# Optimization experiments

Hardware: AMD Instinct MI355X
Metric: run time of the kernel (lower is better)

The kernel has to match this reference:

```python
import jax, jax.numpy as jnp
import numpy as np

N_NODES = 50000
N_EDGES = 1600000
SLOPE = 0.01  # torch leaky_relu default negative_slope


def _lrelu(x):
    return jnp.where(x >= 0, x, SLOPE * x)


def _graph_conv(x, edge_index, w_rel, b_rel, w_root):
    # PyG GraphConv (aggr='add'): out_i = W_rel @ sum_{j->i} x_j + b_rel + W_root @ x_i
    src, dst = edge_index[0], edge_index[1]
    agg = jax.ops.segment_sum(x[src], dst, num_segments=x.shape[0])  # [N, F_in]
    return agg @ w_rel.T + b_rel + x @ w_root.T


def setup_inputs() -> dict:
    key = jax.random.key(0)
    ks = jax.random.split(key, 12)

    def glorot(k, shape):
        fan_in = shape[-1]
        return jax.random.normal(k, shape, dtype=jnp.float32) / np.sqrt(fan_in)

    x = jax.random.normal(ks[0], (N_NODES, 2048), dtype=jnp.float32)
    edge_index = jax.random.randint(ks[1], (2, N_EDGES), 0, N_NODES, dtype=jnp.int64)

    return {
        "x": x,
        "edge_index": edge_index,
        "lin1_w": glorot(ks[2], (128, 2048)),
        "lin1_b": jnp.zeros((128,), jnp.float32),
        "conv1_w_rel": glorot(ks[3], (64, 128)),
        "conv1_b_rel": jnp.zeros((64,), jnp.float32),
        "conv1_w_root": glorot(ks[4], (64, 128)),
        "conv4_w_rel": glorot(ks[5], (32, 64)),
        "conv4_b_rel": jnp.zeros((32,), jnp.float32),
        "conv4_w_root": glorot(ks[6], (32, 64)),
        "pos_w": glorot(ks[7], (3, 32)),
        "pos_b": jnp.zeros((3,), jnp.float32),
    }


def reference(x, edge_index, lin1_w, lin1_b, conv1_w_rel, conv1_b_rel,
              conv1_w_root, conv4_w_rel, conv4_b_rel, conv4_w_root,
              pos_w, pos_b):
    # dropout layers are identity at inference
    h = _lrelu(x @ lin1_w.T + lin1_b)                                  # [N, 128]
    h = _lrelu(_graph_conv(h, edge_index, conv1_w_rel, conv1_b_rel, conv1_w_root))  # [N, 64]
    h = _lrelu(_graph_conv(h, edge_index, conv4_w_rel, conv4_b_rel, conv4_w_root))  # [N, 32]
    position = h @ pos_w.T + pos_b                                     # [N, 3]
    return position
```

## Files before the change

### kernel.cpp

```cpp
#include <hip/hip_runtime.h>

#define N_NODES 50000
#define N_EDGES 1600000
#define LIN_BLOCKS 782
#define HIST_BLOCKS 1024

typedef __attribute__((ext_vector_type(4))) float f32x4;
typedef __attribute__((ext_vector_type(8))) short bf16x8;
typedef unsigned short u16;

__device__ __forceinline__ float lrelu(float x) { return x >= 0.f ? x : 0.01f * x; }

__device__ __forceinline__ u16 f2bf(float f) {
    union { float f; unsigned u; } v; v.f = f;
    unsigned u = v.u;
    u += 0x7fffu + ((u >> 16) & 1u);
    return (u16)(u >> 16);
}

__device__ __forceinline__ float bf2f(u16 v) {
    union { unsigned u; float f; } x; x.u = ((unsigned)v) << 16; return x.f;
}

__device__ __forceinline__ bf16x8 cvt8(float4 a, float4 b) {
    bf16x8 r;
    r[0] = (short)f2bf(a.x); r[1] = (short)f2bf(a.y);
    r[2] = (short)f2bf(a.z); r[3] = (short)f2bf(a.w);
    r[4] = (short)f2bf(b.x); r[5] = (short)f2bf(b.y);
    r[6] = (short)f2bf(b.z); r[7] = (short)f2bf(b.w);
    return r;
}

__launch_bounds__(256)
__global__ void k_prep(const float* __restrict__ W1,
                       const float* __restrict__ W2a, const float* __restrict__ W2b,
                       const float* __restrict__ W3a, const float* __restrict__ W3b,
                       u16* __restrict__ wf1, u16* __restrict__ wf2, u16* __restrict__ wf3,
                       const int* __restrict__ ei, int* __restrict__ deg)
{
    const int b = blockIdx.x;
    if (b < 1024) {
        int i = b * 256 + threadIdx.x;
        int e = i & 7, lane = (i >> 3) & 63, nf = (i >> 9) & 7, ks = i >> 12;
        int n = nf * 16 + (lane & 15);
        int k = ks * 32 + 8 * (lane >> 4) + e;
        wf1[i] = f2bf(W1[(size_t)n * 2048 + k]);
    } else if (b < 1088) {
        int i = (b - 1024) * 256 + threadIdx.x;
        int e = i & 7, lane = (i >> 3) & 63, nf = (i >> 9) & 7, ks = i >> 12;
        int n = nf * 16 + (lane & 15);
        int k = ks * 32 + 8 * (lane >> 4) + e;
        float v = (n < 64) ? W2a[(size_t)n * 128 + k] : W2b[(size_t)(n - 64) * 128 + k];
        wf2[i] = f2bf(v);
    } else if (b < 1104) {
        int i = (b - 1088) * 256 + threadIdx.x;
        int e = i & 7, lane = (i >> 3) & 63, nf = (i >> 9) & 3, ks = i >> 11;
        int n = nf * 16 + (lane & 15);
        int k = ks * 32 + 8 * (lane >> 4) + e;
        float v = (n < 32) ? W3a[(size_t)n * 64 + k] : W3b[(size_t)(n - 32) * 64 + k];
        wf3[i] = f2bf(v);
    } else {
        for (int e = (b - 1104) * 256 + threadIdx.x; e < N_EDGES; e += HIST_BLOCKS * 256)
            atomicAdd(deg + ei[N_EDGES + e], 1);
    }
}

__device__ __forceinline__ void wr_stage(char* slot, int aw0, int aw1, int bw,
                                         float4 A0, float4 A1, float4 B0, float4 B1)
{
    *(float4*)(slot + aw0) = A0;
    *(float4*)(slot + aw1) = A1;
    *(float4*)(slot + bw) = B0;
    *(float4*)(slot + bw + 16) = B1;
}

__device__ __forceinline__ void compute_step(const char* slot, int lane, int wave,
                                             f32x4 acc[8])
{
    const int lrow = lane & 15, lgrp = lane >> 4;
    const int row = wave * 16 + lrow;
    const int swz = (row & 7) << 4;
    const char* Ab = slot + row * 128;
    float4 a0 = *(const float4*)(Ab + ((lgrp * 32) ^ swz));
    float4 a1 = *(const float4*)(Ab + ((lgrp * 32 + 16) ^ swz));
    bf16x8 af = cvt8(a0, a1);
    const char* Bb = slot + 8192 + lane * 16;
    __builtin_amdgcn_s_setprio(1);
#pragma unroll
    for (int nf = 0; nf < 8; nf++) {
        bf16x8 bf = *(const bf16x8*)(Bb + nf * 1024);
        acc[nf] = __builtin_amdgcn_mfma_f32_16x16x32_bf16(af, bf, acc[nf], 0, 0, 0);
    }
    __builtin_amdgcn_s_setprio(0);
}

__launch_bounds__(256, 3)
__global__ void k_linf(const float* __restrict__ X, const u16* __restrict__ Wf1,
                       const u16* __restrict__ Wf2,
                       const float* __restrict__ Bv, const float* __restrict__ brel,
                       u16* __restrict__ t1, float* __restrict__ acc1,
                       const int* __restrict__ ei, int* __restrict__ cur,
                       int* __restrict__ csr)
{
    __shared__ __align__(16) char lds[2][16384];
    __shared__ __align__(16) u16 hlbuf[4][2048];

    const int t = threadIdx.x, wave = t >> 6, lane = t & 63;
    const int lrow = lane & 15, lgrp = lane >> 4;
    const int m0 = blockIdx.x * 64;

    const int arow_l = t >> 2, q = t & 3;
    int grow = m0 + arow_l; if (grow >= N_NODES) grow = N_NODES - 1;
    const float4* ap = (const float4*)(X + (size_t)grow * 2048);
    const float4* bp = (const float4*)Wf1;
    const int aw0 = arow_l * 128 + (((q * 2 + 0) ^ (arow_l & 7)) << 4);
    const int aw1 = arow_l * 128 + (((q * 2 + 1) ^ (arow_l & 7)) << 4);
    const int bw = 8192 + t * 32;

    f32x4 acc[8];
#pragma unroll
    for (int i = 0; i < 8; i++) acc[i] = (f32x4)0.f;

    float4 cA0 = ap[q * 2], cA1 = ap[q * 2 + 1];
    float4 cB0 = bp[t * 2], cB1 = bp[t * 2 + 1];
    float4 nA0 = ap[8 + q * 2], nA1 = ap[8 + q * 2 + 1];
    float4 nB0 = bp[512 + t * 2], nB1 = bp[512 + t * 2 + 1];
    wr_stage(lds[0], aw0, aw1, bw, cA0, cA1, cB0, cB1);
    asm volatile("s_waitcnt lgkmcnt(0)" ::: "memory");
    __builtin_amdgcn_s_barrier();
    __builtin_amdgcn_sched_barrier(0);

#pragma unroll 2
    for (int s = 0; s < 62; s++) {
        float4 fA0 = ap[(s + 2) * 8 + q * 2], fA1 = ap[(s + 2) * 8 + q * 2 + 1];
        float4 fB0 = bp[(s + 2) * 512 + t * 2], fB1 = bp[(s + 2) * 512 + t * 2 + 1];

        compute_step(lds[s & 1], lane, wave, acc);
        __builtin_amdgcn_s_barrier();
        __builtin_amdgcn_sched_barrier(0);

        wr_stage(lds[(s + 1) & 1], aw0, aw1, bw, nA0, nA1, nB0, nB1);
        asm volatile("s_waitcnt lgkmcnt(0)" ::: "memory");
        __builtin_amdgcn_s_barrier();
        __builtin_amdgcn_sched_barrier(0);

        nA0 = fA0; nA1 = fA1; nB0 = fB0; nB1 = fB1;
    }
    compute_step(lds[0], lane, wave, acc);
    __builtin_amdgcn_s_barrier();
    __builtin_amdgcn_sched_barrier(0);
    wr_stage(lds[1], aw0, aw1, bw, nA0, nA1, nB0, nB1);
    asm volatile("s_waitcnt lgkmcnt(0)" ::: "memory");
    __builtin_amdgcn_s_barrier();
    __builtin_amdgcn_sched_barrier(0);
    compute_step(lds[1], lane, wave, acc);

    u16* hl = hlbuf[wave];
#pragma unroll
    for (int nf = 0; nf < 8; nf++) {
        const int col = nf * 16 + lrow;
        const float bias = Bv[col];
#pragma unroll
        for (int r = 0; r < 4; r++) {
            const int row = lgrp * 4 + r;
            hl[row * 128 + (((col >> 3) ^ (row & 7)) << 3) + (col & 7)] =
                f2bf(lrelu(acc[nf][r] + bias));
        }
    }
    bf16x8 af2[4];
#pragma unroll
    for (int ks = 0; ks < 4; ks++)
        af2[ks] = *(const bf16x8*)(hl + lrow * 128 + ((((ks << 2) + lgrp) ^ (lrow & 7)) << 3));

    f32x4 dacc[8];
#pragma unroll
    for (int i = 0; i < 8; i++) dacc[i] = (f32x4)0.f;
    const u16* bp2 = Wf2 + lane * 8;
#pragma unroll
    for (int ks = 0; ks < 4; ks++) {
#pragma unroll
        for (int nf = 0; nf < 8; nf++) {
            bf16x8 bf = *(const bf16x8*)(bp2 + ks * 4096 + nf * 512);
            dacc[nf] = __builtin_amdgcn_mfma_f32_16x16x32_bf16(af2[ks], bf, dacc[nf], 0, 0, 0);
        }
    }

    const int rbase = m0 + wave * 16 + lgrp * 4;
#pragma unroll
    for (int nf = 0; nf < 8; nf++) {
        const int col = nf * 16 + lrow;
#pragma unroll
        for (int r = 0; r < 4; r++) {
            const int row = rbase + r;
            if (row < N_NODES) {
                if (col < 64) t1[(size_t)row * 64 + col] = f2bf(dacc[nf][r]);
                else          acc1[(size_t)row * 64 + (col - 64)] = dacc[nf][r] + brel[col - 64];
            }
        }
    }

    for (int e = blockIdx.x * 256 + t; e < N_EDGES; e += LIN_BLOCKS * 256) {
        const int dst = ei[N_EDGES + e];
        const int p = atomicAdd(cur + dst, 1);
        csr[p] = ei[e];
    }
}

__launch_bounds__(256, 2)
__global__ void k_dualf2(const float* __restrict__ A, const u16* __restrict__ Wf,
                         const float* __restrict__ brel,
                         u16* __restrict__ t2, float* __restrict__ acc2)
{
    const int t = threadIdx.x, wave = t >> 6, lane = t & 63;
    const int lrow = lane & 15, lgrp = lane >> 4;
    const int arow = blockIdx.x * 64 + wave * 16 + lrow;
    const float* ap = A + (size_t)(arow < N_NODES ? arow : 0) * 64 + 8 * lgrp;
    const u16* bp = Wf + lane * 8;

    float4 a00 = *(const float4*)(ap + 0);
    float4 a01 = *(const float4*)(ap + 4);
    float4 a10 = *(const float4*)(ap + 32);
    float4 a11 = *(const float4*)(ap + 36);

    f32x4 acc[4];
#pragma unroll
    for (int i = 0; i < 4; i++) acc[i] = (f32x4)0.f;

    a00.x = lrelu(a00.x); a00.y = lrelu(a00.y); a00.z = lrelu(a00.z); a00.w = lrelu(a00.w);
    a01.x = lrelu(a01.x); a01.y = lrelu(a01.y); a01.z = lrelu(a01.z); a01.w = lrelu(a01.w);
    bf16x8 af0 = cvt8(a00, a01);
    a10.x = lrelu(a10.x); a10.y = lrelu(a10.y); a10.z = lrelu(a10.z); a10.w = lrelu(a10.w);
    a11.x = lrelu(a11.x); a11.y = lrelu(a11.y); a11.z = lrelu(a11.z); a11.w = lrelu(a11.w);
    bf16x8 af1 = cvt8(a10, a11);

#pragma unroll
    for (int nf = 0; nf < 4; nf++) {
        bf16x8 b0 = *(const bf16x8*)(bp + nf * 512);
        bf16x8 b1 = *(const bf16x8*)(bp + 2048 + nf * 512);
        acc[nf] = __builtin_amdgcn_mfma_f32_16x16x32_bf16(af0, b0, acc[nf], 0, 0, 0);
        acc[nf] = __builtin_amdgcn_mfma_f32_16x16x32_bf16(af1, b1, acc[nf], 0, 0, 0);
    }

    const int rbase = blockIdx.x * 64 + wave * 16 + lgrp * 4;
#pragma unroll
    for (int nf = 0; nf < 4; nf++) {
        const int col = nf * 16 + lrow;
#pragma unroll
        for (int r = 0; r < 4; r++) {
            const int row = rbase + r;
            if (row < N_NODES) {
                if (col < 32) t2[(size_t)row * 32 + col] = f2bf(acc[nf][r]);
                else          acc2[(size_t)row * 32 + (col - 32)] = acc[nf][r] + brel[col - 32];
            }
        }
    }
}

__launch_bounds__(256)
__global__ void k_scan1(const int* __restrict__ deg, int* __restrict__ tmp,
                        int* __restrict__ bsum)
{
    __shared__ int sm[256];
    const int tid = threadIdx.x;
    const int i = blockIdx.x * 256 + tid;
    int d = (i < N_NODES) ? deg[i] : 0;
    sm[tid] = d;
    __syncthreads();
#pragma unroll
    for (int off = 1; off < 256; off <<= 1) {
        int v = (tid >= off) ? sm[tid - off] : 0;
        __syncthreads();
        sm[tid] += v;
        __syncthreads();
    }
    if (i < N_NODES) tmp[i] = sm[tid];
    if (tid == 255) bsum[blockIdx.x] = sm[255];
}

__launch_bounds__(256)
__global__ void k_scan2p(const int* __restrict__ bsum, int* __restrict__ boff, int nb)
{
    __shared__ int sm[256];
    const int tid = threadIdx.x;
    int v = (tid < nb) ? bsum[tid] : 0;
    sm[tid] = v;
    __syncthreads();
#pragma unroll
    for (int off = 1; off < 256; off <<= 1) {
        int u = (tid >= off) ? sm[tid - off] : 0;
        __syncthreads();
        sm[tid] += u;
        __syncthreads();
    }
    if (tid < nb) boff[tid] = sm[tid] - v;
}

__launch_bounds__(256)
__global__ void k_scan3(const int* __restrict__ tmp, const int* __restrict__ boff,
                        const int* __restrict__ deg, int* __restrict__ ro,
                        int* __restrict__ cur)
{
    const int i = blockIdx.x * 256 + threadIdx.x;
    if (i < N_NODES) {
        int incl = tmp[i] + boff[i >> 8];
        ro[i + 1] = incl;
        cur[i] = incl - deg[i];
    }
    if (i == 0) ro[0] = 0;
}

__launch_bounds__(256)
__global__ void k_gather64(const int* __restrict__ ro, const int* __restrict__ csr,
                           const u16* __restrict__ t, float* __restrict__ acc)
{
    const int wid = (blockIdx.x << 2) | (threadIdx.x >> 6);
    if (wid >= N_NODES) return;
    const int lane = threadIdx.x & 63;
    const int s = ro[wid], e = ro[wid + 1];
    float a = acc[(size_t)wid * 64 + lane];
    int i = s;
    for (; i + 8 <= e; i += 8) {
        int s0 = csr[i], s1 = csr[i + 1], s2 = csr[i + 2], s3 = csr[i + 3];
        int s4 = csr[i + 4], s5 = csr[i + 5], s6 = csr[i + 6], s7 = csr[i + 7];
        u16 v0 = t[(size_t)s0 * 64 + lane], v1 = t[(size_t)s1 * 64 + lane];
        u16 v2 = t[(size_t)s2 * 64 + lane], v3 = t[(size_t)s3 * 64 + lane];
        u16 v4 = t[(size_t)s4 * 64 + lane], v5 = t[(size_t)s5 * 64 + lane];
        u16 v6 = t[(size_t)s6 * 64 + lane], v7 = t[(size_t)s7 * 64 + lane];
        a += bf2f(v0); a += bf2f(v1); a += bf2f(v2); a += bf2f(v3);
        a += bf2f(v4); a += bf2f(v5); a += bf2f(v6); a += bf2f(v7);
    }
    for (; i < e; ++i) a += bf2f(t[(size_t)csr[i] * 64 + lane]);
    acc[(size_t)wid * 64 + lane] = a;
}

__launch_bounds__(256)
__global__ void k_gpos(const int* __restrict__ ro, const int* __restrict__ csr,
                       const u16* __restrict__ t, const float* __restrict__ acc2,
                       const float* __restrict__ PW, const float* __restrict__ PB,
                       float* __restrict__ out)
{
    const int wid = (blockIdx.x << 2) | (threadIdx.x >> 6);
    if (wid >= N_NODES) return;
    const int lane = threadIdx.x & 63;
    const int half = lane >> 5, f = lane & 31;
    const int s = ro[wid], e = ro[wid + 1];
    float a = 0.f;
    int i = s;
    for (; i + 8 <= e; i += 8) {
        int s0 = csr[i + half], s1 = csr[i + 2 + half];
        int s2 = csr[i + 4 + half], s3 = csr[i + 6 + half];
        u16 v0 = t[(size_t)s0 * 32 + f], v1 = t[(size_t)s1 * 32 + f];
        u16 v2 = t[(size_t)s2 * 32 + f], v3 = t[(size_t)s3 * 32 + f];
        a += bf2f(v0); a += bf2f(v1); a += bf2f(v2); a += bf2f(v3);
    }
    for (; i < e; i += 2) {
        int idx = i + half;
        if (idx < e) a += bf2f(t[(size_t)csr[idx] * 32 + f]);
    }
    a += __shfl_xor(a, 32, 64);

    float v = lrelu(acc2[(size_t)wid * 32 + f] + a);
    float p0 = v * PW[f], p1 = v * PW[32 + f], p2 = v * PW[64 + f];
#pragma unroll
    for (int off = 16; off >= 1; off >>= 1) {
        p0 += __shfl_xor(p0, off, 64);
        p1 += __shfl_xor(p1, off, 64);
        p2 += __shfl_xor(p2, off, 64);
    }
    if (lane == 0) {
        out[(size_t)wid * 3 + 0] = p0 + PB[0];
        out[(size_t)wid * 3 + 1] = p1 + PB[1];
        out[(size_t)wid * 3 + 2] = p2 + PB[2];
    }
}

extern "C" void kernel_launch(void* const* d_in, const int* in_sizes, int n_in,
                              void* d_out, int out_size, void* d_ws, size_t ws_size,
                              hipStream_t stream)
{
    const float* x        = (const float*)d_in[0];
    const int*   ei       = (const int*)d_in[1];
    const float* lin1_w   = (const float*)d_in[2];
    const float* lin1_b   = (const float*)d_in[3];
    const float* c1_wrel  = (const float*)d_in[4];
    const float* c1_brel  = (const float*)d_in[5];
    const float* c1_wroot = (const float*)d_in[6];
    const float* c4_wrel  = (const float*)d_in[7];
    const float* c4_brel  = (const float*)d_in[8];
    const float* c4_wroot = (const float*)d_in[9];
    const float* pos_w    = (const float*)d_in[10];
    const float* pos_b    = (const float*)d_in[11];
    float* out = (float*)d_out;

    char* base = (char*)d_ws;
    u16*   t1b  = (u16*)base;
    float* acc1 = (float*)(base + 6400000);
    u16*   t2b  = (u16*)(base + 19200000);
    float* acc2 = (float*)(base + 22400000);
    u16*   wf1  = (u16*)(base + 28800000);
    u16*   wf2  = wf1 + 262144;
    u16*   wf3  = wf2 + 16384;
    int*   ibase = (int*)(wf3 + 4096);
    const int NPAD = ((N_NODES + 255) / 256) * 256;
    int* deg  = ibase;
    int* tmp  = deg  + NPAD;
    int* ro   = tmp  + NPAD;
    int* cur  = ro   + NPAD;
    int* bsum = cur  + NPAD;
    int* boff = bsum + 256;
    int* csr  = boff + 256;
    const int NB = (N_NODES + 255) / 256;

    hipMemsetAsync(deg, 0, (size_t)NPAD * sizeof(int), stream);
    hipLaunchKernelGGL(k_prep, dim3(1104 + HIST_BLOCKS), dim3(256), 0, stream,
                       lin1_w, c1_wrel, c1_wroot, c4_wrel, c4_wroot,
                       wf1, wf2, wf3, ei, deg);
    hipLaunchKernelGGL(k_scan1, dim3(NB), dim3(256), 0, stream, deg, tmp, bsum);
    hipLaunchKernelGGL(k_scan2p, dim3(1), dim3(256), 0, stream, bsum, boff, NB);
    hipLaunchKernelGGL(k_scan3, dim3(NB), dim3(256), 0, stream, tmp, boff, deg, ro, cur);

    hipLaunchKernelGGL(k_linf, dim3(LIN_BLOCKS), dim3(256), 0, stream,
                       x, wf1, wf2, lin1_b, c1_brel, t1b, acc1, ei, cur, csr);
    hipLaunchKernelGGL(k_gather64, dim3((N_NODES + 3) / 4), dim3(256), 0, stream,
                       ro, csr, t1b, acc1);
    hipLaunchKernelGGL(k_dualf2, dim3((N_NODES + 63) / 64), dim3(256), 0, stream,
                       acc1, wf3, c4_brel, t2b, acc2);
    hipLaunchKernelGGL(k_gpos, dim3((N_NODES + 3) / 4), dim3(256), 0, stream,
                       ro, csr, t2b, acc2, pos_w, pos_b, out);
}
```

Before: 369.7 us.

## Stage bf16 operands in LDS and retile waves to 32x64 output blocks

The first GEMM now converts X tiles to bf16 before writing them to LDS, and copies the pre-converted bf16 weights into LDS as-is rather than as float. This halves LDS footprint per stage and moves the conversion out of the compute step. Each wave now computes a 32x64 sub-tile (2 A fragments by 4 B fragments) instead of 16x128, which cuts per-wave B-fragment LDS reads. The epilogue reuses the staging LDS for the hidden tile, with an extra barrier since waves exchange rows. Lower LDS use allows raising launch bounds occupancy from 3 to 4 blocks.

After: 361.4 us. 1.02x faster.

```diff
diff --git a/kernel.cpp b/kernel.cpp
--- a/kernel.cpp
+++ b/kernel.cpp
@@ -65,36 +65,35 @@
     }
 }
 
-__device__ __forceinline__ void wr_stage(char* slot, int aw0, int aw1, int bw,
-                                         float4 A0, float4 A1, float4 B0, float4 B1)
-{
-    *(float4*)(slot + aw0) = A0;
-    *(float4*)(slot + aw1) = A1;
-    *(float4*)(slot + bw) = B0;
-    *(float4*)(slot + bw + 16) = B1;
-}
-
 __device__ __forceinline__ void compute_step(const char* slot, int lane, int wave,
-                                             f32x4 acc[8])
-{
-    const int lrow = lane & 15, lgrp = lane >> 4;
-    const int row = wave * 16 + lrow;
-    const int swz = (row & 7) << 4;
-    const char* Ab = slot + row * 128;
-    float4 a0 = *(const float4*)(Ab + ((lgrp * 32) ^ swz));
-    float4 a1 = *(const float4*)(Ab + ((lgrp * 32 + 16) ^ swz));
-    bf16x8 af = cvt8(a0, a1);
-    const char* Bb = slot + 8192 + lane * 16;
+                                             f32x4 acc[2][4])
+{
+    const int lrow = lane & 15;
+    const int k16 = lane >> 4;
+    const int nfb = (wave >> 1) << 2;
+    const int rb = (wave & 1) << 5;
+
+    bf16x8 af[2];
+#pragma unroll
+    for (int st = 0; st < 2; st++) {
+        const int row = rb + st * 16 + lrow;
+        af[st] = *(const bf16x8*)(slot + row * 64 + ((k16 ^ (row & 3)) << 4));
+    }
+    bf16x8 bf[4];
+#pragma unroll
+    for (int j = 0; j < 4; j++)
+        bf[j] = *(const bf16x8*)(slot + 4096 + (nfb + j) * 1024 + lane * 16);
+
     __builtin_amdgcn_s_setprio(1);
 #pragma unroll
-    for (int nf = 0; nf < 8; nf++) {
-        bf16x8 bf = *(const bf16x8*)(Bb + nf * 1024);
-        acc[nf] = __builtin_amdgcn_mfma_f32_16x16x32_bf16(af, bf, acc[nf], 0, 0, 0);
-    }
+    for (int st = 0; st < 2; st++)
+#pragma unroll
+        for (int j = 0; j < 4; j++)
+            acc[st][j] = __builtin_amdgcn_mfma_f32_16x16x32_bf16(af[st], bf[j], acc[st][j], 0, 0, 0);
     __builtin_amdgcn_s_setprio(0);
 }
 
-__launch_bounds__(256, 3)
+__launch_bounds__(256, 4)
 __global__ void k_linf(const float* __restrict__ X, const u16* __restrict__ Wf1,
                        const u16* __restrict__ Wf2,
                        const float* __restrict__ Bv, const float* __restrict__ brel,
@@ -102,44 +101,49 @@
                        const int* __restrict__ ei, int* __restrict__ cur,
                        int* __restrict__ csr)
 {
-    __shared__ __align__(16) char lds[2][16384];
-    __shared__ __align__(16) u16 hlbuf[4][2048];
+    __shared__ __align__(16) char lds[2][12288];
 
     const int t = threadIdx.x, wave = t >> 6, lane = t & 63;
     const int lrow = lane & 15, lgrp = lane >> 4;
     const int m0 = blockIdx.x * 64;
 
-    const int arow_l = t >> 2, q = t & 3;
+    const int arow_l = t >> 2, kq = t & 3;
     int grow = m0 + arow_l; if (grow >= N_NODES) grow = N_NODES - 1;
     const float4* ap = (const float4*)(X + (size_t)grow * 2048);
-    const float4* bp = (const float4*)Wf1;
-    const int aw0 = arow_l * 128 + (((q * 2 + 0) ^ (arow_l & 7)) << 4);
-    const int aw1 = arow_l * 128 + (((q * 2 + 1) ^ (arow_l & 7)) << 4);
-    const int bw = 8192 + t * 32;
-
-    f32x4 acc[8];
-#pragma unroll
-    for (int i = 0; i < 8; i++) acc[i] = (f32x4)0.f;
-
-    float4 cA0 = ap[q * 2], cA1 = ap[q * 2 + 1];
-    float4 cB0 = bp[t * 2], cB1 = bp[t * 2 + 1];
-    float4 nA0 = ap[8 + q * 2], nA1 = ap[8 + q * 2 + 1];
-    float4 nB0 = bp[512 + t * 2], nB1 = bp[512 + t * 2 + 1];
-    wr_stage(lds[0], aw0, aw1, bw, cA0, cA1, cB0, cB1);
+    const bf16x8* bp = (const bf16x8*)Wf1;
+    const int awr = arow_l * 64 + ((kq ^ (arow_l & 3)) << 4);
+    const int bwr = 4096 + t * 32;
+
+    f32x4 acc[2][4];
+#pragma unroll
+    for (int st = 0; st < 2; st++)
+#pragma unroll
+        for (int j = 0; j < 4; j++) acc[st][j] = (f32x4)0.f;
+
+    float4 cA0 = ap[kq * 2], cA1 = ap[kq * 2 + 1];
+    bf16x8 cB0 = bp[t * 2], cB1 = bp[t * 2 + 1];
+    float4 nA0 = ap[8 + kq * 2], nA1 = ap[8 + kq * 2 + 1];
+    bf16x8 nB0 = bp[512 + t * 2], nB1 = bp[512 + t * 2 + 1];
+    *(bf16x8*)(lds[0] + awr) = cvt8(cA0, cA1);
+    *(bf16x8*)(lds[0] + bwr) = cB0;
+    *(bf16x8*)(lds[0] + bwr + 16) = cB1;
     asm volatile("s_waitcnt lgkmcnt(0)" ::: "memory");
     __builtin_amdgcn_s_barrier();
     __builtin_amdgcn_sched_barrier(0);
 
 #pragma unroll 2
     for (int s = 0; s < 62; s++) {
-        float4 fA0 = ap[(s + 2) * 8 + q * 2], fA1 = ap[(s + 2) * 8 + q * 2 + 1];
-        float4 fB0 = bp[(s + 2) * 512 + t * 2], fB1 = bp[(s + 2) * 512 + t * 2 + 1];
+        float4 fA0 = ap[(s + 2) * 8 + kq * 2], fA1 = ap[(s + 2) * 8 + kq * 2 + 1];
+        bf16x8 fB0 = bp[(s + 2) * 512 + t * 2], fB1 = bp[(s + 2) * 512 + t * 2 + 1];
 
         compute_step(lds[s & 1], lane, wave, acc);
         __builtin_amdgcn_s_barrier();
         __builtin_amdgcn_sched_barrier(0);
 
-        wr_stage(lds[(s + 1) & 1], aw0, aw1, bw, nA0, nA1, nB0, nB1);
+        char* wslot = lds[(s + 1) & 1];
+        *(bf16x8*)(wslot + awr) = cvt8(nA0, nA1);
+        *(bf16x8*)(wslot + bwr) = nB0;
+        *(bf16x8*)(wslot + bwr + 16) = nB1;
         asm volatile("s_waitcnt lgkmcnt(0)" ::: "memory");
         __builtin_amdgcn_s_barrier();
         __builtin_amdgcn_sched_barrier(0);
@@ -149,29 +153,47 @@
     compute_step(lds[0], lane, wave, acc);
     __builtin_amdgcn_s_barrier();
     __builtin_amdgcn_sched_barrier(0);
-    wr_stage(lds[1], aw0, aw1, bw, nA0, nA1, nB0, nB1);
+    *(bf16x8*)(lds[1] + awr) = cvt8(nA0, nA1);
+    *(bf16x8*)(lds[1] + bwr) = nB0;
+    *(bf16x8*)(lds[1] + bwr + 16) = nB1;
     asm volatile("s_waitcnt lgkmcnt(0)" ::: "memory");
     __builtin_amdgcn_s_barrier();
     __builtin_amdgcn_sched_barrier(0);
     compute_step(lds[1], lane, wave, acc);
-
-    u16* hl = hlbuf[wave];
-#pragma unroll
-    for (int nf = 0; nf < 8; nf++) {
-        const int col = nf * 16 + lrow;
-        const float bias = Bv[col];
-#pragma unroll
-        for (int r = 0; r < 4; r++) {
-            const int row = lgrp * 4 + r;
-            hl[row * 128 + (((col >> 3) ^ (row & 7)) << 3) + (col & 7)] =
-                f2bf(lrelu(acc[nf][r] + bias));
+    __builtin_amdgcn_s_barrier();
+    __builtin_amdgcn_sched_barrier(0);
+
+    u16* hl = (u16*)&lds[0][0];
+    {
+        const int nfb = (wave >> 1) << 2, rb = (wave & 1) << 5;
+#pragma unroll
+        for (int st = 0; st < 2; st++) {
+#pragma unroll
+            for (int j = 0; j < 4; j++) {
+                const int col = nfb * 16 + j * 16 + lrow;
+                const float bias = Bv[col];
+#pragma unroll
+                for (int r = 0; r < 4; r++) {
+                    const int row = rb + st * 16 + lgrp * 4 + r;
+                    hl[row * 128 + (((col >> 3) ^ (row & 7)) << 3) + (col & 7)] =
+                        f2bf(lrelu(acc[st][j][r] + bias));
+                }
+            }
         }
     }
+    asm volatile("s_waitcnt lgkmcnt(0)" ::: "memory");
+    __builtin_amdgcn_s_barrier();
+    __builtin_amdgcn_sched_barrier(0);
+
     bf16x8 af2[4];
-#pragma unroll
-    for (int ks = 0; ks < 4; ks++)
-        af2[ks] = *(const bf16x8*)(hl + lrow * 128 + ((((ks << 2) + lgrp) ^ (lrow & 7)) << 3));
-
+    {
+        const int row = wave * 16 + lrow;
+#pragma unroll
+        for (int ks = 0; ks < 4; ks++) {
+            const int chunk = ((ks << 2) + lgrp) ^ (row & 7);
+            af2[ks] = *(const bf16x8*)(hl + row * 128 + (chunk << 3));
+        }
+    }
     f32x4 dacc[8];
 #pragma unroll
     for (int i = 0; i < 8; i++) dacc[i] = (f32x4)0.f;
```

## Drop LDS staging in linear GEMM; load A and B directly into registers

Applied to the files above, without the earlier changes.

The first linear layer's GEMM no longer stages X and W tiles through double-buffered shared memory with barriers. Each wave loads its own 16 rows of X straight from global memory with a 4-deep register prefetch ring, and reads pre-swizzled bf16 weight fragments directly from global memory (relying on L2/L1 caching). Freeing 32KB of LDS and removing barriers lets launch bounds rise to 4 blocks per SM. The cost is that every wave now reads the weight tile from cache on its own, and there is no cooperative, coalesced staging.

New measurement: 454.0 us. 1.23x slower.

```diff
diff --git a/kernel.cpp b/kernel.cpp
--- a/kernel.cpp
+++ b/kernel.cpp
@@ -65,36 +65,7 @@
     }
 }
 
-__device__ __forceinline__ void wr_stage(char* slot, int aw0, int aw1, int bw,
-                                         float4 A0, float4 A1, float4 B0, float4 B1)
-{
-    *(float4*)(slot + aw0) = A0;
-    *(float4*)(slot + aw1) = A1;
-    *(float4*)(slot + bw) = B0;
-    *(float4*)(slot + bw + 16) = B1;
-}
-
-__device__ __forceinline__ void compute_step(const char* slot, int lane, int wave,
-                                             f32x4 acc[8])
-{
-    const int lrow = lane & 15, lgrp = lane >> 4;
-    const int row = wave * 16 + lrow;
-    const int swz = (row & 7) << 4;
-    const char* Ab = slot + row * 128;
-    float4 a0 = *(const float4*)(Ab + ((lgrp * 32) ^ swz));
-    float4 a1 = *(const float4*)(Ab + ((lgrp * 32 + 16) ^ swz));
-    bf16x8 af = cvt8(a0, a1);
-    const char* Bb = slot + 8192 + lane * 16;
-    __builtin_amdgcn_s_setprio(1);
-#pragma unroll
-    for (int nf = 0; nf < 8; nf++) {
-        bf16x8 bf = *(const bf16x8*)(Bb + nf * 1024);
-        acc[nf] = __builtin_amdgcn_mfma_f32_16x16x32_bf16(af, bf, acc[nf], 0, 0, 0);
-    }
-    __builtin_amdgcn_s_setprio(0);
-}
-
-__launch_bounds__(256, 3)
+__launch_bounds__(256, 4)
 __global__ void k_linf(const float* __restrict__ X, const u16* __restrict__ Wf1,
                        const u16* __restrict__ Wf2,
                        const float* __restrict__ Bv, const float* __restrict__ brel,
@@ -102,58 +73,42 @@
                        const int* __restrict__ ei, int* __restrict__ cur,
                        int* __restrict__ csr)
 {
-    __shared__ __align__(16) char lds[2][16384];
     __shared__ __align__(16) u16 hlbuf[4][2048];
 
     const int t = threadIdx.x, wave = t >> 6, lane = t & 63;
     const int lrow = lane & 15, lgrp = lane >> 4;
     const int m0 = blockIdx.x * 64;
 
-    const int arow_l = t >> 2, q = t & 3;
-    int grow = m0 + arow_l; if (grow >= N_NODES) grow = N_NODES - 1;
-    const float4* ap = (const float4*)(X + (size_t)grow * 2048);
-    const float4* bp = (const float4*)Wf1;
-    const int aw0 = arow_l * 128 + (((q * 2 + 0) ^ (arow_l & 7)) << 4);
-    const int aw1 = arow_l * 128 + (((q * 2 + 1) ^ (arow_l & 7)) << 4);
-    const int bw = 8192 + t * 32;
+    int arow = m0 + wave * 16 + lrow;
+    if (arow >= N_NODES) arow = N_NODES - 1;
+    const float4* ap = (const float4*)(X + (size_t)arow * 2048 + lgrp * 8);
+    const bf16x8* bp = (const bf16x8*)Wf1 + lane;
 
     f32x4 acc[8];
 #pragma unroll
     for (int i = 0; i < 8; i++) acc[i] = (f32x4)0.f;
 
-    float4 cA0 = ap[q * 2], cA1 = ap[q * 2 + 1];
-    float4 cB0 = bp[t * 2], cB1 = bp[t * 2 + 1];
-    float4 nA0 = ap[8 + q * 2], nA1 = ap[8 + q * 2 + 1];
-    float4 nB0 = bp[512 + t * 2], nB1 = bp[512 + t * 2 + 1];
-    wr_stage(lds[0], aw0, aw1, bw, cA0, cA1, cB0, cB1);
-    asm volatile("s_waitcnt lgkmcnt(0)" ::: "memory");
-    __builtin_amdgcn_s_barrier();
-    __builtin_amdgcn_sched_barrier(0);
-
-#pragma unroll 2
-    for (int s = 0; s < 62; s++) {
-        float4 fA0 = ap[(s + 2) * 8 + q * 2], fA1 = ap[(s + 2) * 8 + q * 2 + 1];
-        float4 fB0 = bp[(s + 2) * 512 + t * 2], fB1 = bp[(s + 2) * 512 + t * 2 + 1];
-
-        compute_step(lds[s & 1], lane, wave, acc);
-        __builtin_amdgcn_s_barrier();
-        __builtin_amdgcn_sched_barrier(0);
-
-        wr_stage(lds[(s + 1) & 1], aw0, aw1, bw, nA0, nA1, nB0, nB1);
-        asm volatile("s_waitcnt lgkmcnt(0)" ::: "memory");
-        __builtin_amdgcn_s_barrier();
-        __builtin_amdgcn_sched_barrier(0);
-
-        nA0 = fA0; nA1 = fA1; nB0 = fB0; nB1 = fB1;
-    }
-    compute_step(lds[0], lane, wave, acc);
-    __builtin_amdgcn_s_barrier();
-    __builtin_amdgcn_sched_barrier(0);
-    wr_stage(lds[1], aw0, aw1, bw, nA0, nA1, nB0, nB1);
-    asm volatile("s_waitcnt lgkmcnt(0)" ::: "memory");
-    __builtin_amdgcn_s_barrier();
-    __builtin_amdgcn_sched_barrier(0);
-    compute_step(lds[1], lane, wave, acc);
+    float4 a0[4], a1[4];
+#pragma unroll
+    for (int p = 0; p < 4; p++) { a0[p] = ap[p * 8]; a1[p] = ap[p * 8 + 1]; }
+
+#pragma unroll 4
+    for (int s = 0; s < 64; s++) {
+        bf16x8 af = cvt8(a0[s & 3], a1[s & 3]);
+        const int pf = (s + 4 < 64) ? (s + 4) : 63;
+        a0[s & 3] = ap[pf * 8];
+        a1[s & 3] = ap[pf * 8 + 1];
+
+        const bf16x8* b = bp + s * 512;
+        acc[0] = __builtin_amdgcn_mfma_f32_16x16x32_bf16(af, b[0 * 64], acc[0], 0, 0, 0);
+        acc[1] = __builtin_amdgcn_mfma_f32_16x16x32_bf16(af, b[1 * 64], acc[1], 0, 0, 0);
+        acc[2] = __builtin_amdgcn_mfma_f32_16x16x32_bf16(af, b[2 * 64], acc[2], 0, 0, 0);
+        acc[3] = __builtin_amdgcn_mfma_f32_16x16x32_bf16(af, b[3 * 64], acc[3], 0, 0, 0);
+        acc[4] = __builtin_amdgcn_mfma_f32_16x16x32_bf16(af, b[4 * 64], acc[4], 0, 0, 0);
+        acc[5] = __builtin_amdgcn_mfma_f32_16x16x32_bf16(af, b[5 * 64], acc[5], 0, 0, 0);
+        acc[6] = __builtin_amdgcn_mfma_f32_16x16x32_bf16(af, b[6 * 64], acc[6], 0, 0, 0);
+        acc[7] = __builtin_amdgcn_mfma_f32_16x16x32_bf16(af, b[7 * 64], acc[7], 0, 0, 0);
+    }
 
     u16* hl = hlbuf[wave];
 #pragma unroll
@@ -167,6 +122,8 @@
                 f2bf(lrelu(acc[nf][r] + bias));
         }
     }
+    asm volatile("s_waitcnt lgkmcnt(0)" ::: "memory");
+
     bf16x8 af2[4];
 #pragma unroll
     for (int ks = 0; ks < 4; ks++)
```
